# Kernel optimization log

Measured on AMD Instinct MI355X. Metric: run time of the kernel, lower is better.

The kernel has to match this reference:

```python
import jax, jax.numpy as jnp
import numpy as np

NUM_NODES = 25
EMBED_DIM = 64
OUT_SIZE = 2
N_TOTAL = 204800   # 8192 graphs * 25 nodes
N_EDGES = 3276800  # avg degree 16


def setup_inputs() -> dict:
    key = jax.random.key(0)
    ks = jax.random.split(key, 8)
    x = jax.random.normal(ks[0], (N_TOTAL, EMBED_DIM), dtype=jnp.float32)
    # random edges; real graphs are graph-local but math is identical
    edge_index = jax.random.randint(ks[1], (2, N_EDGES), 0, N_TOTAL, dtype=jnp.int32)
    batch = jnp.repeat(jnp.arange(N_TOTAL // NUM_NODES, dtype=jnp.int32), NUM_NODES)
    hid = NUM_NODES * EMBED_DIM  # 1600
    W_conv = jax.random.normal(ks[2], (EMBED_DIM, EMBED_DIM), dtype=jnp.float32) / np.sqrt(EMBED_DIM)
    b_conv = jnp.zeros((EMBED_DIM,), dtype=jnp.float32)
    W1 = jax.random.normal(ks[3], (hid, hid), dtype=jnp.float32) / np.sqrt(hid)
    b1 = jnp.zeros((hid,), dtype=jnp.float32)
    W2 = jax.random.normal(ks[4], (hid, OUT_SIZE), dtype=jnp.float32) / np.sqrt(hid)
    b2 = jnp.zeros((OUT_SIZE,), dtype=jnp.float32)
    return {"x": x, "edge_index": edge_index, "batch": batch,
            "W_conv": W_conv, "b_conv": b_conv,
            "W1": W1, "b1": b1, "W2": W2, "b2": b2}


def reference(x, edge_index, batch, W_conv, b_conv, W1, b1, W2, b2):
    N = x.shape[0]
    # --- GCNConv: add self-loops, symmetric degree norm, transform, scatter-add ---
    loop = jnp.arange(N, dtype=edge_index.dtype)
    src = jnp.concatenate([edge_index[0], loop])
    dst = jnp.concatenate([edge_index[1], loop])
    deg = jax.ops.segment_sum(jnp.ones_like(dst, dtype=x.dtype), dst, num_segments=N)
    dinv = jax.lax.rsqrt(deg)  # deg >= 1 due to self-loops
    norm = dinv[src] * dinv[dst]                       # [E+N]
    h = x @ W_conv                                     # [N, D]
    msg = h[src] * norm[:, None]                       # gather + scale
    h = jax.ops.segment_sum(msg, dst, num_segments=N) + b_conv
    h = jax.nn.relu(h)
    # --- dense head ---
    nb = -(-batch.shape[0] // NUM_NODES)               # ceil
    h = h.reshape(nb, NUM_NODES * EMBED_DIM)           # [B, 1600]
    h = jax.nn.relu(h @ W1 + b1)
    logits = h @ W2 + b2
    return jax.nn.softmax(logits, axis=-1)
```

## Files before the change

### kernel.cpp

```cpp
#include <hip/hip_runtime.h>
#include <hip/hip_bf16.h>
#include <stdint.h>

#define NT   204800
#define NE   3276800
#define ED   64
#define NBG  8192
#define HID  1600
#define CAP  56
#define NBKT 400
#define BCAP 9216

typedef float  f32x4  __attribute__((ext_vector_type(4)));
typedef __bf16 bf16x8 __attribute__((ext_vector_type(8)));

__device__ __forceinline__ void async_ld16(const void* g, void* l) {
    __builtin_amdgcn_global_load_lds(
        (__attribute__((address_space(1))) const void*)g,
        (__attribute__((address_space(3))) void*)l, 16, 0, 0);
}

__device__ __forceinline__ unsigned short f2bf_raw(float f) {
    __hip_bfloat16 h = __float2bfloat16(f);
    return *(unsigned short*)&h;
}

__global__ void k_initg(int* __restrict__ gcur) {
    int t = threadIdx.x;
    if (t < NBKT) gcur[t] = t * BCAP;
}

__global__ __launch_bounds__(256) void k_part(const int* __restrict__ srcv,
                                              const int* __restrict__ dstv,
                                              int* __restrict__ gcur,
                                              unsigned* __restrict__ rec) {
    __shared__ int hist[NBKT];
    __shared__ int gofs[NBKT];
    const int t = threadIdx.x;
    const int base = blockIdx.x * (NE / 512);
    for (int i = t; i < NBKT; i += 256) hist[i] = 0;
    __syncthreads();
    unsigned keep[25];
#pragma unroll
    for (int j = 0; j < 25; ++j) {
        int d = dstv[base + j * 256 + t];
        int b = d >> 9;
        int ls = atomicAdd(&hist[b], 1);
        keep[j] = ((unsigned)ls << 18) | ((unsigned)(d & 511) << 9) | (unsigned)b;
    }
    __syncthreads();
    for (int i = t; i < NBKT; i += 256) gofs[i] = atomicAdd(&gcur[i], hist[i]);
    __syncthreads();
#pragma unroll
    for (int j = 0; j < 25; ++j) {
        int s = srcv[base + j * 256 + t];
        unsigned k = keep[j];
        int b   = (int)(k & 511u);
        int rel = (int)((k >> 9) & 511u);
        int idx = gofs[b] + (int)(k >> 18);
        if (idx < (b + 1) * BCAP)
            rec[idx] = ((unsigned)s << 9) | (unsigned)rel;
    }
}

__global__ __launch_bounds__(512) void k_fillb(const int* __restrict__ gcur,
                                               const unsigned* __restrict__ rec,
                                               int* __restrict__ cur,
                                               int* __restrict__ csr,
                                               float* __restrict__ dinv) {
    __shared__ int cnt[512];
    const int t = threadIdx.x;
    const int b = blockIdx.x;
    const int n0 = b * 512;
    cnt[t] = 0;
    __syncthreads();
    const int bstart = b * BCAP;
    int bcnt = gcur[b] - bstart;
    bcnt = (bcnt > BCAP) ? BCAP : bcnt;
    for (int idx = t; idx < bcnt; idx += 512) {
        unsigned r = rec[bstart + idx];
        unsigned rel = r & 511u;
        int ls = atomicAdd(&cnt[rel], 1);
        if (ls < CAP) csr[(size_t)(n0 + rel) * CAP + ls] = (int)(r >> 9);
    }
    __syncthreads();
    int cn = cnt[t];
    cur[n0 + t] = cn;
    dinv[n0 + t] = rsqrtf((float)cn + 1.f);
}

__global__ __launch_bounds__(256) void k_gemm_conv(const float* __restrict__ x,
                                                   const float* __restrict__ Wc,
                                                   const float* __restrict__ dinv,
                                                   __hip_bfloat16* __restrict__ hbs) {
    __shared__ unsigned short Xs[64 * 72];
    __shared__ unsigned short Wt[64 * 72];
    const int t = threadIdx.x;
    const int row0 = blockIdx.x * 64;
#pragma unroll
    for (int i = 0; i < 4; ++i) {
        int idx = i * 256 + t;
        int r = idx >> 4, c4 = (idx & 15) << 2;
        f32x4 wv = ((const f32x4*)Wc)[idx];
        Wt[(c4 + 0) * 72 + r] = f2bf_raw(wv.x);
        Wt[(c4 + 1) * 72 + r] = f2bf_raw(wv.y);
        Wt[(c4 + 2) * 72 + r] = f2bf_raw(wv.z);
        Wt[(c4 + 3) * 72 + r] = f2bf_raw(wv.w);
        f32x4 xv = ((const f32x4*)(x + (size_t)row0 * 64))[idx];
        ushort4 p;
        p.x = f2bf_raw(xv.x);
        p.y = f2bf_raw(xv.y);
        p.z = f2bf_raw(xv.z);
        p.w = f2bf_raw(xv.w);
        *(ushort4*)&Xs[r * 72 + c4] = p;
    }
    __syncthreads();
    const int w = t >> 6, lane = t & 63;
    const int fr = lane & 15, fq = lane >> 4;
    f32x4 acc[4] = {};
#pragma unroll
    for (int kb = 0; kb < 2; ++kb) {
        bf16x8 av = *(const bf16x8*)&Xs[(w * 16 + fr) * 72 + kb * 32 + fq * 8];
#pragma unroll
        for (int j = 0; j < 4; ++j) {
            bf16x8 bv = *(const bf16x8*)&Wt[(j * 16 + fr) * 72 + kb * 32 + fq * 8];
            acc[j] = __builtin_amdgcn_mfma_f32_16x16x32_bf16(av, bv, acc[j], 0, 0, 0);
        }
    }
#pragma unroll
    for (int r = 0; r < 4; ++r) {
        int row = row0 + w * 16 + fq * 4 + r;
        float di = dinv[row];
        unsigned short* dst = (unsigned short*)&hbs[(size_t)row * 64];
#pragma unroll
        for (int j = 0; j < 4; ++j)
            dst[j * 16 + fr] = f2bf_raw(acc[j][r] * di);
    }
}

__global__ __launch_bounds__(256) void k_gather(const int* __restrict__ cur,
                                                const int* __restrict__ csr,
                                                const float* __restrict__ dinv,
                                                const __hip_bfloat16* __restrict__ hbs,
                                                const float* __restrict__ bc,
                                                __hip_bfloat16* __restrict__ Hb) {
    const int lane = threadIdx.x & 63;
    const int du = __builtin_amdgcn_readfirstlane(blockIdx.x * 4 + (threadIdx.x >> 6));
    const float di = dinv[du];
    int cn = cur[du];
    cn = (cn > CAP) ? CAP : cn;
    const int* __restrict__ lst = csr + (size_t)du * CAP;
    const float self = __bfloat162float(hbs[(size_t)du * ED + lane]);
    float acc = self;
    int e = 0;
    for (; e + 16 <= cn; e += 16) {
#pragma unroll
        for (int q = 0; q < 16; ++q) {
            int s = lst[e + q];
            acc += __bfloat162float(hbs[(size_t)s * ED + lane]);
        }
    }
    if (e < cn) {
        const int pad = e + 16 - cn;
#pragma unroll
        for (int q = 0; q < 16; ++q) {
            int s = (e + q < cn) ? lst[e + q] : du;
            acc += __bfloat162float(hbs[(size_t)s * ED + lane]);
        }
        acc = fmaf(-(float)pad, self, acc);
    }
    Hb[(size_t)du * ED + lane] = __float2bfloat16(fmaxf(bc[lane] + di * acc, 0.f));
}

__global__ void k_convW1(const float* __restrict__ W1, __hip_bfloat16* __restrict__ Bt) {
    __shared__ float tile[64][65];
    const int t = threadIdx.x;
    const int k0 = blockIdx.x * 64;
    const int n0 = blockIdx.y * 64;
#pragma unroll
    for (int i = 0; i < 16; ++i) {
        int lin = i * 256 + t;
        int r = lin >> 6, c = lin & 63;
        tile[r][c] = W1[(size_t)(k0 + r) * HID + n0 + c];
    }
    __syncthreads();
#pragma unroll
    for (int i = 0; i < 16; ++i) {
        int lin = i * 256 + t;
        int nn = lin >> 6, kk = lin & 63;
        Bt[(size_t)(n0 + nn) * HID + k0 + kk] = __float2bfloat16(tile[kk][nn]);
    }
}

__global__ __launch_bounds__(128) void k_gemm1(const __hip_bfloat16* __restrict__ A,
                                               const __hip_bfloat16* __restrict__ Bt,
                                               const float* __restrict__ b1,
                                               __hip_bfloat16* __restrict__ h2) {
    __shared__ unsigned short As[2][128 * 64];
    __shared__ unsigned short Bs[2][64 * 64];
    const int t = threadIdx.x;
    const int lane = t & 63;
    const int w = t >> 6;
    const int lin = blockIdx.x;
    const int xc  = lin & 7;
    const int pos = lin >> 3;
    const int bm0 = (xc * 8 + (pos & 7)) * 128;
    const int bn0 = (pos >> 3) * 64;
    const int fr = lane & 15;
    const int fq = lane >> 4;
    const int lrow  = lane >> 3;
    const int lslot = (lane & 7) ^ lrow;
    const size_t soff = (size_t)lrow * HID + lslot * 8;
    const __hip_bfloat16* pa = A  + (size_t)bm0 * HID + soff;
    const __hip_bfloat16* pb = Bt + (size_t)bn0 * HID + soff;
    const int ra  = (w * 64 + fr) * 64;
    const int rb  = fr * 64;
    const int sl0 = ((0 + fq) ^ (fr & 7)) * 8;
    const int sl1 = ((4 + fq) ^ (fr & 7)) * 8;
    f32x4 acc[4][4] = {};

    auto STAGE = [&](int bidx) {
        unsigned short* dA = &As[bidx][(w * 8) * 512 + lane * 8];
        const __hip_bfloat16* sA = pa + (size_t)(w * 8) * 8 * HID;
#pragma unroll
        for (int q = 0; q < 8; ++q)
            async_ld16(sA + (size_t)q * 8 * HID, dA + q * 512);
        unsigned short* dB = &Bs[bidx][(w * 4) * 512 + lane * 8];
        const __hip_bfloat16* sB = pb + (size_t)(w * 4) * 8 * HID;
#pragma unroll
        for (int q = 0; q < 4; ++q)
            async_ld16(sB + (size_t)q * 8 * HID, dB + q * 512);
        pa += 64; pb += 64;
    };

    const int NKT = HID / 64;
    STAGE(0);
    STAGE(1);
    for (int kt = 0; kt < NKT; ++kt) {
        const int p = kt & 1;
        if (kt < NKT - 1)
            asm volatile("s_waitcnt vmcnt(12)\n\ts_barrier" ::: "memory");
        else
            asm volatile("s_waitcnt vmcnt(0)\n\ts_barrier" ::: "memory");
        bf16x8 av0[4], av1[4], bv0[4], bv1[4];
#pragma unroll
        for (int i = 0; i < 4; ++i) {
            av0[i] = *(const bf16x8*)&As[p][ra + i * 16 * 64 + sl0];
            av1[i] = *(const bf16x8*)&As[p][ra + i * 16 * 64 + sl1];
        }
#pragma unroll
        for (int j = 0; j < 4; ++j) {
            bv0[j] = *(const bf16x8*)&Bs[p][rb + j * 16 * 64 + sl0];
            bv1[j] = *(const bf16x8*)&Bs[p][rb + j * 16 * 64 + sl1];
        }
#pragma unroll
        for (int i = 0; i < 4; ++i)
#pragma unroll
            for (int j = 0; j < 4; ++j) {
                acc[i][j] = __builtin_amdgcn_mfma_f32_16x16x32_bf16(av0[i], bv0[j], acc[i][j], 0, 0, 0);
                acc[i][j] = __builtin_amdgcn_mfma_f32_16x16x32_bf16(av1[i], bv1[j], acc[i][j], 0, 0, 0);
            }
        if (kt < NKT - 2) {
            asm volatile("s_waitcnt lgkmcnt(0)\n\ts_barrier" ::: "memory");
            STAGE(p);
        }
    }

#pragma unroll
    for (int j = 0; j < 4; ++j) {
        int n = bn0 + j * 16 + fr;
        float bias = b1[n];
#pragma unroll
        for (int i = 0; i < 4; ++i) {
#pragma unroll
            for (int r = 0; r < 4; ++r) {
                int m = bm0 + w * 64 + i * 16 + fq * 4 + r;
                float v = acc[i][j][r] + bias;
                h2[(size_t)m * HID + n] = __float2bfloat16(fmaxf(v, 0.f));
            }
        }
    }
}

__global__ void k_head(const __hip_bfloat16* __restrict__ h2, const float* __restrict__ W2,
                       const float* __restrict__ b2, float* __restrict__ out) {
    int g = blockIdx.x * 4 + (threadIdx.x >> 6);
    int lane = threadIdx.x & 63;
    const __hip_bfloat16* row = h2 + (size_t)g * HID;
    float a0 = 0.f, a1 = 0.f;
#pragma unroll
    for (int i = 0; i < 25; ++i) {
        int k = i * 64 + lane;
        float hv = __bfloat162float(row[k]);
        float2 w = ((const float2*)W2)[k];
        a0 += hv * w.x;
        a1 += hv * w.y;
    }
#pragma unroll
    for (int off = 32; off > 0; off >>= 1) {
        a0 += __shfl_down(a0, off, 64);
        a1 += __shfl_down(a1, off, 64);
    }
    if (lane == 0) {
        float l0 = a0 + b2[0], l1 = a1 + b2[1];
        float mx = fmaxf(l0, l1);
        float e0 = expf(l0 - mx), e1 = expf(l1 - mx);
        float s = e0 + e1;
        out[2 * g]     = e0 / s;
        out[2 * g + 1] = e1 / s;
    }
}

extern "C" void kernel_launch(void* const* d_in, const int* in_sizes, int n_in,
                              void* d_out, int out_size, void* d_ws, size_t ws_size,
                              hipStream_t stream) {
    const float* x  = (const float*)d_in[0];
    const int*   ei = (const int*)d_in[1];
    const float* Wc = (const float*)d_in[3];
    const float* bc = (const float*)d_in[4];
    const float* W1 = (const float*)d_in[5];
    const float* b1 = (const float*)d_in[6];
    const float* W2 = (const float*)d_in[7];
    const float* b2 = (const float*)d_in[8];
    float* out = (float*)d_out;

    const int* srcv = ei;
    const int* dstv = ei + NE;

    char* ws = (char*)d_ws;
    int*   cur  = (int*)ws;
    float* dinv = (float*)(ws + 819200);
    int*   gcur = (int*)(ws + 1638400);
    int*   csr  = (int*)(ws + 1642496);
    unsigned* rec = (unsigned*)(ws + 47517696);
    __hip_bfloat16* hbs = (__hip_bfloat16*)(ws + 47517696);
    __hip_bfloat16* h2  = (__hip_bfloat16*)(ws + 47517696);
    __hip_bfloat16* Hb  = (__hip_bfloat16*)(ws + 73732096);
    __hip_bfloat16* Bt  = (__hip_bfloat16*)(ws + 99946496);

    k_initg    <<<1, 512, 0, stream>>>(gcur);
    k_part     <<<512, 256, 0, stream>>>(srcv, dstv, gcur, rec);
    k_fillb    <<<NBKT, 512, 0, stream>>>(gcur, rec, cur, csr, dinv);
    k_gemm_conv<<<NT / 64, 256, 0, stream>>>(x, Wc, dinv, hbs);
    k_gather   <<<NT / 4, 256, 0, stream>>>(cur, csr, dinv, hbs, bc, Hb);
    k_convW1   <<<dim3(HID / 64, HID / 64), 256, 0, stream>>>(W1, Bt);
    k_gemm1    <<<1600, 128, 0, stream>>>(Hb, Bt, b1, h2);
    k_head     <<<NBG / 4, 256, 0, stream>>>(h2, W2, b2, out);
}
```

Baseline: 377.6 us.

## Stage partition and CSR writes in LDS for coalesced global stores

The partition kernel now computes a per-block prefix scan of bucket histograms, reorders records into shared memory by bucket, and then writes them to global memory in contiguous runs instead of scattered single-word stores. The CSR fill kernel is split into two half-bucket blocks that build each 256-node CSR slab in LDS and copy it out with vectorized 16-byte stores. Both changes aim to replace random uncoalesced global writes with coalesced ones. The cost is extra LDS traffic and syncs, a log-step scan, a large LDS footprint (~57KB) in k_fillb that limits occupancy, and each fill block reading its whole bucket to keep only half of it.

```diff
diff --git a/kernel.cpp b/kernel.cpp
--- a/kernel.cpp
+++ b/kernel.cpp
@@ -10,9 +10,11 @@
 #define CAP  56
 #define NBKT 400
 #define BCAP 9216
+#define EPB  (NE / 512)
 
 typedef float  f32x4  __attribute__((ext_vector_type(4)));
 typedef __bf16 bf16x8 __attribute__((ext_vector_type(8)));
+typedef int    i32x4  __attribute__((ext_vector_type(4)));
 
 __device__ __forceinline__ void async_ld16(const void* g, void* l) {
     __builtin_amdgcn_global_load_lds(
@@ -35,9 +37,13 @@
                                               int* __restrict__ gcur,
                                               unsigned* __restrict__ rec) {
     __shared__ int hist[NBKT];
+    __shared__ int scanA[NBKT];
+    __shared__ int scanB[NBKT];
     __shared__ int gofs[NBKT];
-    const int t = threadIdx.x;
-    const int base = blockIdx.x * (NE / 512);
+    __shared__ unsigned buf[EPB];
+    __shared__ unsigned short bkt[EPB];
+    const int t = threadIdx.x;
+    const int base = blockIdx.x * EPB;
     for (int i = t; i < NBKT; i += 256) hist[i] = 0;
     __syncthreads();
     unsigned keep[25];
@@ -50,6 +56,16 @@
     }
     __syncthreads();
     for (int i = t; i < NBKT; i += 256) gofs[i] = atomicAdd(&gcur[i], hist[i]);
+    for (int i = t; i < NBKT; i += 256) scanA[i] = hist[i];
+    __syncthreads();
+    int* sp = scanA; int* dp = scanB;
+    for (int off = 1; off < NBKT; off <<= 1) {
+        for (int i = t; i < NBKT; i += 256)
+            dp[i] = sp[i] + ((i >= off) ? sp[i - off] : 0);
+        __syncthreads();
+        int* tmp = sp; sp = dp; dp = tmp;
+    }
+    for (int i = t; i < NBKT; i += 256) dp[i] = sp[i] - hist[i];
     __syncthreads();
 #pragma unroll
     for (int j = 0; j < 25; ++j) {
@@ -57,33 +73,49 @@
         unsigned k = keep[j];
         int b   = (int)(k & 511u);
         int rel = (int)((k >> 9) & 511u);
-        int idx = gofs[b] + (int)(k >> 18);
+        int ls  = (int)(k >> 18);
+        int li  = dp[b] + ls;
+        buf[li] = ((unsigned)s << 9) | (unsigned)rel;
+        bkt[li] = (unsigned short)b;
+    }
+    __syncthreads();
+    for (int i = t; i < EPB; i += 256) {
+        int b = bkt[i];
+        int idx = gofs[b] + (i - dp[b]);
         if (idx < (b + 1) * BCAP)
-            rec[idx] = ((unsigned)s << 9) | (unsigned)rel;
-    }
-}
-
-__global__ __launch_bounds__(512) void k_fillb(const int* __restrict__ gcur,
+            rec[idx] = buf[i];
+    }
+}
+
+__global__ __launch_bounds__(256) void k_fillb(const int* __restrict__ gcur,
                                                const unsigned* __restrict__ rec,
                                                int* __restrict__ cur,
                                                int* __restrict__ csr,
                                                float* __restrict__ dinv) {
-    __shared__ int cnt[512];
-    const int t = threadIdx.x;
-    const int b = blockIdx.x;
-    const int n0 = b * 512;
+    __shared__ int cnt[256];
+    __shared__ int loc[256 * CAP];
+    const int t = threadIdx.x;
+    const int b = blockIdx.x >> 1;
+    const int h = blockIdx.x & 1;
+    const int n0 = b * 512 + h * 256;
     cnt[t] = 0;
     __syncthreads();
     const int bstart = b * BCAP;
     int bcnt = gcur[b] - bstart;
     bcnt = (bcnt > BCAP) ? BCAP : bcnt;
-    for (int idx = t; idx < bcnt; idx += 512) {
+    for (int idx = t; idx < bcnt; idx += 256) {
         unsigned r = rec[bstart + idx];
-        unsigned rel = r & 511u;
-        int ls = atomicAdd(&cnt[rel], 1);
-        if (ls < CAP) csr[(size_t)(n0 + rel) * CAP + ls] = (int)(r >> 9);
-    }
-    __syncthreads();
+        int rel = (int)(r & 511u);
+        if ((rel >> 8) == h) {
+            int rl = rel & 255;
+            int ls = atomicAdd(&cnt[rl], 1);
+            if (ls < CAP) loc[rl * CAP + ls] = (int)(r >> 9);
+        }
+    }
+    __syncthreads();
+    i32x4* gout = (i32x4*)(csr + (size_t)n0 * CAP);
+    const i32x4* lin = (const i32x4*)loc;
+    for (int i = t; i < 256 * CAP / 4; i += 256) gout[i] = lin[i];
     int cn = cnt[t];
     cur[n0 + t] = cn;
     dinv[n0 + t] = rsqrtf((float)cn + 1.f);
@@ -340,7 +372,7 @@
 
     k_initg    <<<1, 512, 0, stream>>>(gcur);
     k_part     <<<512, 256, 0, stream>>>(srcv, dstv, gcur, rec);
-    k_fillb    <<<NBKT, 512, 0, stream>>>(gcur, rec, cur, csr, dinv);
+    k_fillb    <<<NBKT * 2, 256, 0, stream>>>(gcur, rec, cur, csr, dinv);
     k_gemm_conv<<<NT / 64, 256, 0, stream>>>(x, Wc, dinv, hbs);
     k_gather   <<<NT / 4, 256, 0, stream>>>(cur, csr, dinv, hbs, bc, Hb);
     k_convW1   <<<dim3(HID / 64, HID / 64), 256, 0, stream>>>(W1, Bt);
```

New measurement: 349.2 us. -7.5%, faster.
